# Optimization experiments

Hardware: AMD Instinct MI355X
Metric: run time of the kernel (lower is better)

## Reference

```python
import jax, jax.numpy as jnp
import numpy as np
from jax import lax

K = 8  # diffusion channels
T = 3  # diffusion steps


def setup_inputs() -> dict:
    key = jax.random.key(0)
    k1, k2, k3 = jax.random.split(key, 3)
    x = jax.random.normal(k1, (16, 1, 512, 512), dtype=jnp.float32)
    # per-step conv weights [T, out=k, in=1, kh, kw] and biases [T, k]
    W = jax.random.normal(k2, (T, K, 1, 3, 3), dtype=jnp.float32) * 0.1
    b = jax.random.normal(k3, (T, K), dtype=jnp.float32) * 0.1
    return {"x": x, "W": W, "b": b}


def _g(d):
    # mode 1 edge-stopping function: exp(-|d| / (1 + d^2))
    return jnp.exp(-jnp.abs(d) / (1.0 + d * d))


def reference(x, W, b):
    in_x = x  # [N,1,H,W]
    for t in range(T):
        d1 = lax.conv_general_dilated(
            in_x, W[t], window_strides=(1, 1), padding="SAME",
            dimension_numbers=("NCHW", "OIHW", "NCHW"),
        ) + b[t][None, :, None, None]  # [N,K,H,W]
        features = _g(d1) * d1
        # squash_tensor: sum over the K channels, keep channel dim of 1
        in_x = in_x - jnp.sum(features, axis=1, keepdims=True) / K
    return in_x
```

## Files before the change

kernel.cpp:

```cpp
#include <hip/hip_runtime.h>

static constexpr int IMG   = 512;
static constexpr int TX    = 64;
static constexpr int TY    = 32;
static constexpr int NTHR  = 256;
static constexpr int LSTA  = 72;
static constexpr int LSTB  = 68;
static constexpr int AROWS = 36;
static constexpr int NSTAGE = AROWS * (LSTA / 4);

__device__ __forceinline__ float gd_acc(float d, float acc) {
    const float t    = fmaf(d, d, 1.0f);
    const float rinv = __builtin_amdgcn_rcpf(t);
    const float e    = __builtin_amdgcn_exp2f(
                           -1.442695040888963f * __builtin_fabsf(d) * rinv);
    return fmaf(e, d, acc);
}

__device__ __forceinline__ void ldg8(float* L, const float* __restrict__ img,
                                     int gy, int gx0) {
    float4 a = {0.f,0.f,0.f,0.f}, b = {0.f,0.f,0.f,0.f};
    if ((unsigned)gy < (unsigned)IMG) {
        const float* p = img + gy * IMG;
        if ((unsigned)gx0       < (unsigned)IMG) a = *(const float4*)(p + gx0);
        if ((unsigned)(gx0 + 4) < (unsigned)IMG) b = *(const float4*)(p + gx0 + 4);
    }
    *(float4*)&L[0] = a; *(float4*)&L[4] = b;
}

template<int WOFF, int NR, int RLO, int NG, int ILST, int OLST,
         bool HALOG, bool TO_GLOBAL>
__device__ __forceinline__ void diffuse_step(
    const float* __restrict__ prev, float* __restrict__ cur,
    const float* __restrict__ Wt, const float* __restrict__ bt,
    const float* __restrict__ xin, int xoff, int ty0, int tx0, int tid,
    float* __restrict__ gout)
{
    constexpr int NITEMS = NR * NG;
    for (int idx = tid; idx < NITEMS; idx += NTHR) {
        const int rr = idx / NG, j = idx - rr * NG;
        const int r  = RLO + rr, c0 = 4 * j;

        float L0[8], L1[8], L2[8];
        if (HALOG) {
            const float* bc = prev + (r - 1) * ILST + c0;
            *(float4*)&L1[0] = *(const float4*)(bc);
            *(float4*)&L1[4] = *(const float4*)(bc + 4);
            if (r >= 2) {
                *(float4*)&L0[0] = *(const float4*)(bc - ILST);
                *(float4*)&L0[4] = *(const float4*)(bc - ILST + 4);
            } else {
                ldg8(L0, xin, ty0 - 3, tx0 - 4 + c0);
            }
            if (r <= AROWS - 1) {
                *(float4*)&L2[0] = *(const float4*)(bc + ILST);
                *(float4*)&L2[4] = *(const float4*)(bc + ILST + 4);
            } else {
                ldg8(L2, xin, ty0 + 34, tx0 - 4 + c0);
            }
        } else {
            const float* b0 = prev + (r - 2) * ILST + c0;
            *(float4*)&L0[0] = *(const float4*)(b0);
            *(float4*)&L1[0] = *(const float4*)(b0 + ILST);
            *(float4*)&L2[0] = *(const float4*)(b0 + 2 * ILST);
            *(float2*)&L0[4] = *(const float2*)(b0 + 4);
            *(float2*)&L1[4] = *(const float2*)(b0 + ILST + 4);
            *(float2*)&L2[4] = *(const float2*)(b0 + 2 * ILST + 4);
        }

        float acc[4] = {0.f, 0.f, 0.f, 0.f};
#pragma unroll
        for (int k = 0; k < 8; ++k) {
            const float w0 = Wt[9*k+0], w1 = Wt[9*k+1], w2 = Wt[9*k+2];
            const float w3 = Wt[9*k+3], w4 = Wt[9*k+4], w5 = Wt[9*k+5];
            const float w6 = Wt[9*k+6], w7 = Wt[9*k+7], w8 = Wt[9*k+8];
            const float bk = bt[k];
#pragma unroll
            for (int i = 0; i < 4; ++i) {
                float d = bk;
                d = fmaf(w0, L0[WOFF+i],   d);
                d = fmaf(w1, L0[WOFF+i+1], d);
                d = fmaf(w2, L0[WOFF+i+2], d);
                d = fmaf(w3, L1[WOFF+i],   d);
                d = fmaf(w4, L1[WOFF+i+1], d);
                d = fmaf(w5, L1[WOFF+i+2], d);
                d = fmaf(w6, L2[WOFF+i],   d);
                d = fmaf(w7, L2[WOFF+i+1], d);
                d = fmaf(w8, L2[WOFF+i+2], d);
                acc[i] = gd_acc(d, acc[i]);
            }
        }

        float4 v;
        v.x = L1[WOFF+1] - acc[0] * 0.125f;
        v.y = L1[WOFF+2] - acc[1] * 0.125f;
        v.z = L1[WOFF+3] - acc[2] * 0.125f;
        v.w = L1[WOFF+4] - acc[3] * 0.125f;

        const int gy = ty0 - 3 + r;
        if (TO_GLOBAL) {
            *(float4*)&gout[gy * IMG + tx0 + c0] = v;
        } else {
            const bool ry  = (unsigned)gy < (unsigned)IMG;
            const int  gx0 = xoff + c0;
            v.x = (ry && (unsigned)(gx0 + 0) < (unsigned)IMG) ? v.x : 0.f;
            v.y = (ry && (unsigned)(gx0 + 1) < (unsigned)IMG) ? v.y : 0.f;
            v.z = (ry && (unsigned)(gx0 + 2) < (unsigned)IMG) ? v.z : 0.f;
            v.w = (ry && (unsigned)(gx0 + 3) < (unsigned)IMG) ? v.w : 0.f;
            *(float4*)&cur[(r - 1) * OLST + c0] = v;
        }
    }
}

__global__ __launch_bounds__(NTHR) void deep_ad_fused8(
    const float* __restrict__ x, const float* __restrict__ W,
    const float* __restrict__ b, float* __restrict__ out)
{
    __shared__ float A [AROWS * LSTA];
    __shared__ float Bs[AROWS * LSTB + 2];

    const int tid = threadIdx.x;
    const int tx0 = blockIdx.x * TX;
    const int ty0 = blockIdx.y * TY;
    const float* xin  = x   + (size_t)blockIdx.z * (IMG * IMG);
    float*       gout = out + (size_t)blockIdx.z * (IMG * IMG);

    {
        float4 sv[3];
#pragma unroll
        for (int q = 0; q < 3; ++q) {
            const int item = tid + NTHR * q;
            float4 v = {0.f, 0.f, 0.f, 0.f};
            if (item < NSTAGE) {
                const int rr = item / 18, jj = item - rr * 18;
                const int gy = ty0 - 2 + rr;
                const int gx = tx0 - 4 + 4 * jj;
                if ((unsigned)gy < (unsigned)IMG && (unsigned)gx < (unsigned)IMG)
                    v = *(const float4*)(xin + gy * IMG + gx);
            }
            sv[q] = v;
        }
#pragma unroll
        for (int q = 0; q < 3; ++q) {
            const int item = tid + NTHR * q;
            if (item < NSTAGE) *(float4*)&A[item * 4] = sv[q];
        }
    }
    __syncthreads();

    diffuse_step<1, 36, 1, 17, LSTA, LSTB, true,  false>(
        A,  Bs, W,       b,      xin, tx0 - 2, ty0, tx0, tid, nullptr);
    __syncthreads();
    diffuse_step<0, 34, 2, 17, LSTB, LSTA, false, false>(
        Bs, A,  W + 72,  b + 8,  xin, tx0 - 1, ty0, tx0, tid, nullptr);
    __syncthreads();
    diffuse_step<0, 32, 3, 16, LSTA, 0,    false, true >(
        A, nullptr, W + 144, b + 16, xin, 0, ty0, tx0, tid, gout);
}

extern "C" void kernel_launch(void* const* d_in, const int* in_sizes, int n_in,
                              void* d_out, int out_size, void* d_ws, size_t ws_size,
                              hipStream_t stream)
{
    const float* x = (const float*)d_in[0];
    const float* W = (const float*)d_in[1];
    const float* b = (const float*)d_in[2];
    float* out = (float*)d_out;
    const int N = in_sizes[0] / (IMG * IMG);

    dim3 grid(IMG / TX, IMG / TY, N);
    deep_ad_fused8<<<grid, NTHR, 0, stream>>>(x, W, b, out);
}
```

Before: 133.7 us.

## Split fused diffusion into three per-step register-blocked kernels via workspace

Replaces the single fused three-step kernel (shared-memory tiles with halo recomputation) with three launches of a per-step kernel. Each thread loads 12-wide rows straight from global memory into registers and computes a 4x4 output block, streaming rows through a rolling register buffer. The point is to drop the halo recompute and the shared-memory syncs, at the cost of two extra full-image round trips through global memory (ping-ponging between out and a workspace buffer) and extra launches. The fused kernel is kept as a fallback when the workspace is too small.

After: 131.3 us. No clear change (-1.9%).

```diff
diff --git a/kernel.cpp b/kernel.cpp
--- a/kernel.cpp
+++ b/kernel.cpp
@@ -1,13 +1,6 @@
 #include <hip/hip_runtime.h>
 
-static constexpr int IMG   = 512;
-static constexpr int TX    = 64;
-static constexpr int TY    = 32;
-static constexpr int NTHR  = 256;
-static constexpr int LSTA  = 72;
-static constexpr int LSTB  = 68;
-static constexpr int AROWS = 36;
-static constexpr int NSTAGE = AROWS * (LSTA / 4);
+static constexpr int IMG = 512;
 
 __device__ __forceinline__ float gd_acc(float d, float acc) {
     const float t    = fmaf(d, d, 1.0f);
@@ -16,6 +9,98 @@
                            -1.442695040888963f * __builtin_fabsf(d) * rinv);
     return fmaf(e, d, acc);
 }
+
+__device__ __forceinline__ void load_row12(float* R, const float* __restrict__ src,
+                                           int y, int x0, bool xfast) {
+    const bool rowok = (unsigned)y < (unsigned)IMG;
+    if (xfast && rowok) {
+        const float* p = src + y * IMG + x0 - 4;
+        *(float4*)&R[0] = *(const float4*)(p);
+        *(float4*)&R[4] = *(const float4*)(p + 4);
+        *(float4*)&R[8] = *(const float4*)(p + 8);
+    } else {
+#pragma unroll
+        for (int j = 0; j < 12; ++j) {
+            const int col = x0 - 4 + j;
+            R[j] = (rowok && (unsigned)col < (unsigned)IMG)
+                       ? src[y * IMG + col] : 0.f;
+        }
+    }
+}
+
+__device__ __forceinline__ float4 compute_row(
+    const float* RA, const float* RB, const float* RC,
+    const float* __restrict__ Wt, const float* __restrict__ bt)
+{
+    float acc[4] = {0.f, 0.f, 0.f, 0.f};
+#pragma unroll
+    for (int k = 0; k < 8; ++k) {
+        const float w0 = Wt[9*k+0], w1 = Wt[9*k+1], w2 = Wt[9*k+2];
+        const float w3 = Wt[9*k+3], w4 = Wt[9*k+4], w5 = Wt[9*k+5];
+        const float w6 = Wt[9*k+6], w7 = Wt[9*k+7], w8 = Wt[9*k+8];
+        const float bk = bt[k];
+#pragma unroll
+        for (int i = 0; i < 4; ++i) {
+            float d = bk;
+            d = fmaf(w0, RA[i+3], d);
+            d = fmaf(w1, RA[i+4], d);
+            d = fmaf(w2, RA[i+5], d);
+            d = fmaf(w3, RB[i+3], d);
+            d = fmaf(w4, RB[i+4], d);
+            d = fmaf(w5, RB[i+5], d);
+            d = fmaf(w6, RC[i+3], d);
+            d = fmaf(w7, RC[i+4], d);
+            d = fmaf(w8, RC[i+5], d);
+            acc[i] = gd_acc(d, acc[i]);
+        }
+    }
+    float4 v;
+    v.x = RB[4] - acc[0] * 0.125f;
+    v.y = RB[5] - acc[1] * 0.125f;
+    v.z = RB[6] - acc[2] * 0.125f;
+    v.w = RB[7] - acc[3] * 0.125f;
+    return v;
+}
+
+__global__ __launch_bounds__(256) void ad_step_rb(
+    const float* __restrict__ in, float* __restrict__ outp,
+    const float* __restrict__ Wt, const float* __restrict__ bt)
+{
+    const int tid = threadIdx.x;
+    const int x0  = blockIdx.x * 64 + (tid & 15) * 4;
+    const int y0  = blockIdx.y * 64 + (tid >> 4) * 4;
+    const float* __restrict__ src = in   + (size_t)blockIdx.z * (IMG * IMG);
+    float*       __restrict__ dst = outp + (size_t)blockIdx.z * (IMG * IMG);
+    const bool xfast = (x0 >= 4) && (x0 <= 504);
+
+    float R0[12], R1[12], R2[12], R3[12];
+    load_row12(R0, src, y0 - 1, x0, xfast);
+    load_row12(R1, src, y0,     x0, xfast);
+    load_row12(R2, src, y0 + 1, x0, xfast);
+
+    load_row12(R3, src, y0 + 2, x0, xfast);
+    float4 v0 = compute_row(R0, R1, R2, Wt, bt);
+    *(float4*)&dst[(y0 + 0) * IMG + x0] = v0;
+
+    load_row12(R0, src, y0 + 3, x0, xfast);
+    float4 v1 = compute_row(R1, R2, R3, Wt, bt);
+    *(float4*)&dst[(y0 + 1) * IMG + x0] = v1;
+
+    load_row12(R1, src, y0 + 4, x0, xfast);
+    float4 v2 = compute_row(R2, R3, R0, Wt, bt);
+    *(float4*)&dst[(y0 + 2) * IMG + x0] = v2;
+
+    float4 v3 = compute_row(R3, R0, R1, Wt, bt);
+    *(float4*)&dst[(y0 + 3) * IMG + x0] = v3;
+}
+
+static constexpr int TXF   = 64;
+static constexpr int TYF   = 32;
+static constexpr int NTHR  = 256;
+static constexpr int LSTA  = 72;
+static constexpr int LSTB  = 68;
+static constexpr int AROWS = 36;
+static constexpr int NSTAGE = AROWS * (LSTA / 4);
 
 __device__ __forceinline__ void ldg8(float* L, const float* __restrict__ img,
                                      int gy, int gx0) {
@@ -120,8 +205,8 @@
     __shared__ float Bs[AROWS * LSTB + 2];
 
     const int tid = threadIdx.x;
-    const int tx0 = blockIdx.x * TX;
-    const int ty0 = blockIdx.y * TY;
+    const int tx0 = blockIdx.x * TXF;
+    const int ty0 = blockIdx.y * TYF;
     const float* xin  = x   + (size_t)blockIdx.z * (IMG * IMG);
     float*       gout = out + (size_t)blockIdx.z * (IMG * IMG);
 
@@ -168,6 +253,15 @@
     float* out = (float*)d_out;
     const int N = in_sizes[0] / (IMG * IMG);
 
-    dim3 grid(IMG / TX, IMG / TY, N);
-    deep_ad_fused8<<<grid, NTHR, 0, stream>>>(x, W, b, out);
-}
+    const size_t imgBytes = (size_t)N * IMG * IMG * sizeof(float);
+    if (ws_size >= imgBytes) {
+        float* ws = (float*)d_ws;
+        dim3 g(IMG / 64, IMG / 64, N);
+        ad_step_rb<<<g, 256, 0, stream>>>(x,   out, W + 0,   b + 0);
+        ad_step_rb<<<g, 256, 0, stream>>>(out, ws,  W + 72,  b + 8);
+        ad_step_rb<<<g, 256, 0, stream>>>(ws,  out, W + 144, b + 16);
+    } else {
+        dim3 grid(IMG / TXF, IMG / TYF, N);
+        deep_ad_fused8<<<grid, NTHR, 0, stream>>>(x, W, b, out);
+    }
+}
```

## Split fused diffusion into three per-step kernels using packed FMA

Applied to the files above, without the earlier changes.

Replaces the single fused three-step shared-memory kernel with three separate launches, one per diffusion step. Each launch reads its input directly from global memory and ping-pongs between the output buffer and the workspace, so halo recomputation and shared-memory staging go away. The 3x3 convolution uses packed two-wide float FMA to halve FMA issue count. In exchange it adds two extra full-image global round trips and two extra kernel launches. The fused kernel is kept as a fallback when the workspace is too small.

New measurement: 116.0 us. 13.3% less time.

```diff
diff --git a/kernel.cpp b/kernel.cpp
--- a/kernel.cpp
+++ b/kernel.cpp
@@ -1,8 +1,93 @@
 #include <hip/hip_runtime.h>
 
-static constexpr int IMG   = 512;
-static constexpr int TX    = 64;
-static constexpr int TY    = 32;
+static constexpr int IMG = 512;
+
+typedef float v2f __attribute__((ext_vector_type(2)));
+
+__device__ __forceinline__ v2f pkfma(v2f a, v2f b, v2f c) {
+    return __builtin_elementwise_fma(a, b, c);
+}
+
+__device__ __forceinline__ v2f gd_acc2(v2f d, v2f acc) {
+    const v2f t = pkfma(d, d, (v2f){1.0f, 1.0f});
+    v2f e;
+    e.x = __builtin_amdgcn_exp2f(-1.442695040888963f * __builtin_fabsf(d.x)
+                                 * __builtin_amdgcn_rcpf(t.x));
+    e.y = __builtin_amdgcn_exp2f(-1.442695040888963f * __builtin_fabsf(d.y)
+                                 * __builtin_amdgcn_rcpf(t.y));
+    return pkfma(e, d, acc);
+}
+
+__global__ __launch_bounds__(256) void ad_step_pk(
+    const float* __restrict__ in, float* __restrict__ outp,
+    const float* __restrict__ Wt, const float* __restrict__ bt)
+{
+    const int tid = threadIdx.x;
+    const int x0  = blockIdx.x * 64 + (tid & 15) * 4;
+    const int y   = blockIdx.y * 16 + (tid >> 4);
+    const float* __restrict__ src = in + (size_t)blockIdx.z * (IMG * IMG);
+
+    float L[3][12];
+    const bool xfast = (x0 >= 4) && (x0 <= 504);
+#pragma unroll
+    for (int dy = 0; dy < 3; ++dy) {
+        const int yy = y + dy - 1;
+        const bool rowok = (unsigned)yy < (unsigned)IMG;
+        if (xfast && rowok) {
+            const float* p = src + yy * IMG + x0 - 4;
+            *(float4*)&L[dy][0] = *(const float4*)(p);
+            *(float4*)&L[dy][4] = *(const float4*)(p + 4);
+            *(float4*)&L[dy][8] = *(const float4*)(p + 8);
+        } else {
+#pragma unroll
+            for (int j = 0; j < 12; ++j) {
+                const int col = x0 - 4 + j;
+                L[dy][j] = (rowok && (unsigned)col < (unsigned)IMG)
+                               ? src[yy * IMG + col] : 0.f;
+            }
+        }
+    }
+
+    v2f P[3][5];
+#pragma unroll
+    for (int r = 0; r < 3; ++r)
+#pragma unroll
+        for (int j = 0; j < 5; ++j)
+            P[r][j] = (v2f){L[r][3 + j], L[r][4 + j]};
+
+    v2f acc0 = {0.f, 0.f}, acc1 = {0.f, 0.f};
+#pragma unroll
+    for (int k = 0; k < 8; ++k) {
+        const float w0 = Wt[9*k+0], w1 = Wt[9*k+1], w2 = Wt[9*k+2];
+        const float w3 = Wt[9*k+3], w4 = Wt[9*k+4], w5 = Wt[9*k+5];
+        const float w6 = Wt[9*k+6], w7 = Wt[9*k+7], w8 = Wt[9*k+8];
+        const float bk = bt[k];
+
+        v2f d0 = {bk, bk}, d1 = {bk, bk};
+        d0 = pkfma((v2f){w0, w0}, P[0][0], d0);  d1 = pkfma((v2f){w0, w0}, P[0][2], d1);
+        d0 = pkfma((v2f){w1, w1}, P[0][1], d0);  d1 = pkfma((v2f){w1, w1}, P[0][3], d1);
+        d0 = pkfma((v2f){w2, w2}, P[0][2], d0);  d1 = pkfma((v2f){w2, w2}, P[0][4], d1);
+        d0 = pkfma((v2f){w3, w3}, P[1][0], d0);  d1 = pkfma((v2f){w3, w3}, P[1][2], d1);
+        d0 = pkfma((v2f){w4, w4}, P[1][1], d0);  d1 = pkfma((v2f){w4, w4}, P[1][3], d1);
+        d0 = pkfma((v2f){w5, w5}, P[1][2], d0);  d1 = pkfma((v2f){w5, w5}, P[1][4], d1);
+        d0 = pkfma((v2f){w6, w6}, P[2][0], d0);  d1 = pkfma((v2f){w6, w6}, P[2][2], d1);
+        d0 = pkfma((v2f){w7, w7}, P[2][1], d0);  d1 = pkfma((v2f){w7, w7}, P[2][3], d1);
+        d0 = pkfma((v2f){w8, w8}, P[2][2], d0);  d1 = pkfma((v2f){w8, w8}, P[2][4], d1);
+
+        acc0 = gd_acc2(d0, acc0);
+        acc1 = gd_acc2(d1, acc1);
+    }
+
+    float4 v;
+    v.x = L[1][4] - acc0.x * 0.125f;
+    v.y = L[1][5] - acc0.y * 0.125f;
+    v.z = L[1][6] - acc1.x * 0.125f;
+    v.w = L[1][7] - acc1.y * 0.125f;
+    *(float4*)&outp[(size_t)blockIdx.z * (IMG * IMG) + y * IMG + x0] = v;
+}
+
+static constexpr int TXF   = 64;
+static constexpr int TYF   = 32;
 static constexpr int NTHR  = 256;
 static constexpr int LSTA  = 72;
 static constexpr int LSTB  = 68;
@@ -120,8 +205,8 @@
     __shared__ float Bs[AROWS * LSTB + 2];
 
     const int tid = threadIdx.x;
-    const int tx0 = blockIdx.x * TX;
-    const int ty0 = blockIdx.y * TY;
+    const int tx0 = blockIdx.x * TXF;
+    const int ty0 = blockIdx.y * TYF;
     const float* xin  = x   + (size_t)blockIdx.z * (IMG * IMG);
     float*       gout = out + (size_t)blockIdx.z * (IMG * IMG);
 
@@ -168,6 +253,15 @@
     float* out = (float*)d_out;
     const int N = in_sizes[0] / (IMG * IMG);
 
-    dim3 grid(IMG / TX, IMG / TY, N);
-    deep_ad_fused8<<<grid, NTHR, 0, stream>>>(x, W, b, out);
-}
+    const size_t imgBytes = (size_t)N * IMG * IMG * sizeof(float);
+    if (ws_size >= imgBytes) {
+        float* ws = (float*)d_ws;
+        dim3 g(IMG / 64, IMG / 16, N);
+        ad_step_pk<<<g, 256, 0, stream>>>(x,   out, W + 0,   b + 0);
+        ad_step_pk<<<g, 256, 0, stream>>>(out, ws,  W + 72,  b + 8);
+        ad_step_pk<<<g, 256, 0, stream>>>(ws,  out, W + 144, b + 16);
+    } else {
+        dim3 grid(IMG / TXF, IMG / TYF, N);
+        deep_ad_fused8<<<grid, NTHR, 0, stream>>>(x, W, b, out);
+    }
+}
```
